# Kernel optimization log

Measured on AMD Instinct MI355X. Metric: run time of the kernel, lower is better.

## Reference

```python
import jax, jax.numpy as jnp
import numpy as np

WS = 7            # window_size
P = WS * WS       # tokens per window
NUM_HEADS = 12
N_SCALES = 3      # n_local_region_scales
LOCAL_HEAD = NUM_HEADS // N_SCALES

# relative position index (Swin-style), precomputed as a constant
_coords = np.stack(np.meshgrid(np.arange(WS), np.arange(WS), indexing='ij'))  # (2,WS,WS)
_cf = _coords.reshape(2, -1)                                                  # (2,P)
_rel = (_cf[:, :, None] - _cf[:, None, :]).transpose(1, 2, 0)                 # (P,P,2)
_rel[:, :, 0] += WS - 1
_rel[:, :, 1] += WS - 1
_rel[:, :, 0] *= 2 * WS - 1
REL_IDX = jnp.asarray(_rel.sum(-1))  # (P,P) int


def window_partition(arr, ws):
    # arr: (B, H, W, C) -> (B * H/ws * W/ws, ws, ws, C)
    B, H, W, C = arr.shape
    a = arr.reshape(B, H // ws, ws, W // ws, ws, C)
    return a.transpose(0, 1, 3, 2, 4, 5).reshape(-1, ws, ws, C)


def setup_inputs() -> dict:
    key = jax.random.key(0)
    ks = jax.random.split(key, 4)
    B, H, W, C = 16, 56, 56, 384
    N = H * W
    return {
        'x': jax.random.normal(ks[0], (B, N, C), dtype=jnp.float32),
        'w_qkv': jax.random.normal(ks[1], (C, 3 * C), dtype=jnp.float32) * 0.02,
        'w_proj': jax.random.normal(ks[2], (C, C), dtype=jnp.float32) * 0.02,
        'b_proj': jnp.zeros((C,), dtype=jnp.float32),
        'rel_bias_table': jax.random.normal(ks[3], ((2 * WS - 1) ** 2, LOCAL_HEAD), dtype=jnp.float32) * 0.02,
        'H': H,
        'W': W,
    }


def reference(x, w_qkv, w_proj, b_proj, rel_bias_table, H, W):
    B, N, C = x.shape
    head_dim = C // NUM_HEADS
    local_C = C // N_SCALES
    scale = head_dim ** -0.5

    # qkv projection (no bias), laid out as (3, B, N, C)
    temp = (x @ w_qkv).reshape(B, N, 3, C).transpose(2, 0, 1, 3)

    # relative position bias: (LOCAL_HEAD, P, P)
    bias = rel_bias_table[REL_IDX.reshape(-1)].reshape(P, P, LOCAL_HEAD).transpose(2, 0, 1)

    outs = []
    for i in range(N_SCALES):
        qkv = temp[:, :, :, i * local_C:(i + 1) * local_C]          # (3,B,N,local_C)
        oh, ow = H // (2 ** i), W // (2 ** i)
        n_region = (oh // WS) * (ow // WS)
        qkv = qkv.reshape(3 * B, N, local_C).transpose(0, 2, 1).reshape(3 * B, local_C, H, W)
        if i > 0:
            k = 2 ** i
            r = qkv.reshape(3 * B, local_C, oh, k, ow, k)
            qkv = r.mean(axis=(3, 5)) + r.max(axis=(3, 5))           # avg_pool + max_pool
        qkv = qkv.transpose(0, 2, 3, 1)                              # (3B, oh, ow, local_C)
        qkv = window_partition(qkv, WS)                              # (3B*n_region, WS, WS, local_C)
        qkv = qkv.reshape(3, B, n_region, WS, WS, LOCAL_HEAD, head_dim).transpose(0, 1, 5, 2, 3, 4, 6)
        # NOTE: the original reshapes (B,LOCAL_HEAD,n_region,WS,WS,hd) -> (-1,LOCAL_HEAD,P,hd),
        # which mixes batch/head/region axes; replicated faithfully (row-major reshape).
        q = qkv[0].reshape(-1, LOCAL_HEAD, P, head_dim)
        kk = qkv[1].reshape(-1, LOCAL_HEAD, P, head_dim)
        v = qkv[2].reshape(-1, LOCAL_HEAD, P, head_dim)
        attn = (q * scale) @ jnp.swapaxes(kk, -2, -1) + bias[None]   # (B*R, LH, P, P)
        attn = jax.nn.softmax(attn, axis=-1)
        y = attn @ v                                                 # (B*R, LH, P, hd)
        # faithful inverse of the mixed reshape + (non-inverse) window merge via plain reshape
        y = y.reshape(B, n_region, LOCAL_HEAD, P, head_dim).transpose(0, 2, 4, 1, 3)
        y = y.reshape(B, local_C, oh, ow)
        if i > 0:
            y = jax.image.resize(y, (B, local_C, H, W), method='bilinear')
        y = y.reshape(B, LOCAL_HEAD, head_dim, H, W).transpose(0, 1, 3, 4, 2)  # (B,LH,H,W,hd)
        outs.append(y)

    fused = jnp.concatenate(outs, axis=1)                            # (B,NUM_HEADS,H,W,hd)
    fused = fused.reshape(B, NUM_HEADS, N, C // NUM_HEADS).transpose(0, 2, 1, 3).reshape(B, N, C)
    return fused @ w_proj + b_proj
```

## Files before the change

kernel.cpp:

```cpp
#include <hip/hip_runtime.h>
#include <hip/hip_bf16.h>

typedef __hip_bfloat16 bf16;
typedef __hip_bfloat162 bf16x2;
typedef __attribute__((ext_vector_type(8))) short short8;
typedef __attribute__((ext_vector_type(4))) float f32x4;

__device__ __forceinline__ void storeOut(float* p, float v) { *p = v; }
__device__ __forceinline__ void storeOut(bf16* p, float v) { *p = __float2bfloat16(v); }

#define GLOAD_LDS16(g, l)                                              \
  __builtin_amdgcn_global_load_lds(                                    \
      (const __attribute__((address_space(1))) void*)(g),              \
      (__attribute__((address_space(3))) void*)(l), 16, 0, 0)

__global__ __launch_bounds__(256) void cvt_f32_bf16_kernel(const float* __restrict__ in,
                                                           bf16* __restrict__ out, int n8)
{
  int i = blockIdx.x * 256 + threadIdx.x;
  if (i >= n8) return;
  const float4* p = (const float4*)in + (size_t)i * 2;
  float4 a = p[0], b = p[1];
  union { short8 v; bf16 h[8]; } u;
  u.h[0] = __float2bfloat16(a.x); u.h[1] = __float2bfloat16(a.y);
  u.h[2] = __float2bfloat16(a.z); u.h[3] = __float2bfloat16(a.w);
  u.h[4] = __float2bfloat16(b.x); u.h[5] = __float2bfloat16(b.y);
  u.h[6] = __float2bfloat16(b.z); u.h[7] = __float2bfloat16(b.w);
  *((short8*)out + i) = u.v;
}

__global__ __launch_bounds__(256) void transpose2_kernel(const float* __restrict__ w_qkv,
                                                         const float* __restrict__ w_proj,
                                                         bf16* __restrict__ wqkvT,
                                                         bf16* __restrict__ wprojT)
{
  int idx = blockIdx.x * 256 + threadIdx.x;
  if (idx < 1152 * 384) {
    int n = idx / 384, k = idx - n * 384;
    wqkvT[idx] = __float2bfloat16(w_qkv[(size_t)k * 1152 + n]);
  } else {
    idx -= 1152 * 384;
    int n = idx / 384, k = idx - n * 384;
    wprojT[idx] = __float2bfloat16(w_proj[(size_t)k * 384 + n]);
  }
}

template<typename TC, bool BIAS>
__global__ __launch_bounds__(256) void gemm_mfma(const bf16* __restrict__ A,
                                                 const bf16* __restrict__ Bt,
                                                 const float* __restrict__ bias,
                                                 TC* __restrict__ C,
                                                 int M, int N, int K, int nbx)
{
  __shared__ __align__(16) bf16 As[2][128 * 64];
  __shared__ __align__(16) bf16 Bs[2][128 * 64];
  const int tid = threadIdx.x;
  const int wave = tid >> 6, lane = tid & 63;
  const int cpx = gridDim.x >> 3;
  const int wg = (blockIdx.x & 7) * cpx + (blockIdx.x >> 3);
  const int by = wg / nbx, bx = wg - by * nbx;
  const int bm = by * 128, bn = bx * 128;
  const int wr = wave >> 1, wc = wave & 1;

  f32x4 acc[4][4] = {};

  const bf16* aP[4];
  const bf16* bP[4];
#pragma unroll
  for (int e = 0; e < 4; ++e) {
    int flat = e * 4096 + tid * 16;
    int r = flat >> 7;
    int q = ((flat >> 4) & 7) ^ (r & 7);
    aP[e] = A + (size_t)(bm + r) * K + q * 8;
    bP[e] = Bt + (size_t)(bn + r) * K + q * 8;
  }

  auto STAGE = [&](int buf, int k0) {
    char* aw = (char*)(&As[buf][0]) + wave * 1024;
    char* bw = (char*)(&Bs[buf][0]) + wave * 1024;
#pragma unroll
    for (int e = 0; e < 4; ++e) {
      GLOAD_LDS16(aP[e] + k0, aw + e * 4096);
      GLOAD_LDS16(bP[e] + k0, bw + e * 4096);
    }
  };

  const int lr = lane & 15, lk = lane >> 4;
  const int rbA = (wr * 64 + lr) * 64;
  const int rbB = (wc * 64 + lr) * 64;
  const int q0 = ((lk    ) ^ (lr & 7)) * 8;
  const int q1 = ((4 + lk) ^ (lr & 7)) * 8;

  const int nt = K >> 6;
  STAGE(0, 0);
  int cur = 0;
  for (int t = 0; t < nt; ++t) {
    __syncthreads();
    if (t + 1 < nt) STAGE(cur ^ 1, (t + 1) << 6);
    const bf16* Ab = &As[cur][0];
    const bf16* Bb = &Bs[cur][0];
    short8 af0[4], af1[4], bf0[4], bf1[4];
#pragma unroll
    for (int i = 0; i < 4; ++i) {
      af0[i] = *(const short8*)(Ab + rbA + i * 1024 + q0);
      af1[i] = *(const short8*)(Ab + rbA + i * 1024 + q1);
    }
#pragma unroll
    for (int j = 0; j < 4; ++j) {
      bf0[j] = *(const short8*)(Bb + rbB + j * 1024 + q0);
      bf1[j] = *(const short8*)(Bb + rbB + j * 1024 + q1);
    }
#pragma unroll
    for (int i = 0; i < 4; ++i)
#pragma unroll
      for (int j = 0; j < 4; ++j) {
        acc[i][j] = __builtin_amdgcn_mfma_f32_16x16x32_bf16(af0[i], bf0[j], acc[i][j], 0, 0, 0);
        acc[i][j] = __builtin_amdgcn_mfma_f32_16x16x32_bf16(af1[i], bf1[j], acc[i][j], 0, 0, 0);
      }
    cur ^= 1;
  }

  const int crow = bm + wr * 64 + lk * 4;
  const int ccol = bn + wc * 64 + lr;
#pragma unroll
  for (int j = 0; j < 4; ++j) {
    int col = ccol + j * 16;
    float bv = BIAS ? bias[col] : 0.f;
#pragma unroll
    for (int i = 0; i < 4; ++i)
#pragma unroll
      for (int t = 0; t < 4; ++t) {
        int row = crow + i * 16 + t;
        storeOut(&C[(size_t)row * N + col], acc[i][j][t] + bv);
      }
  }
}

__global__ __launch_bounds__(128) void pool_both_kernel(const bf16* __restrict__ temp,
                                                        bf16* __restrict__ pool1,
                                                        bf16* __restrict__ pool2)
{
  int blk = blockIdx.x;
  bf16* outp; int oh, k, isc;
  if (blk < 3 * 16 * 28 * 28) { outp = pool1; oh = 28; k = 2; isc = 1; }
  else { blk -= 3 * 16 * 28 * 28; outp = pool2; oh = 14; k = 4; isc = 2; }
  const int ow = oh;
  int c = threadIdx.x;
  int x = blk % ow; int t = blk / ow;
  int y = t % oh;  t /= oh;
  int b = t % 16;  int s = t / 16;
  float sum = 0.f, mx = -3.4e38f;
  float inv = 1.0f / (float)(k * k);
  for (int dy = 0; dy < k; ++dy)
    for (int dx = 0; dx < k; ++dx) {
      int h = y * k + dy, w = x * k + dx;
      float v = __bfloat162float(temp[((size_t)b * 3136 + h * 56 + w) * 1152 + s * 384 + isc * 128 + c]);
      sum += v; mx = fmaxf(mx, v);
    }
  outp[((size_t)(s * 16 + b) * oh * ow + y * ow + x) * 128 + c] = __float2bfloat16(sum * inv + mx);
}

struct AttnP {
  const bf16 *qb, *kb, *vb;
  bf16* out;
  int R, Rw, ow, npos, rstride, out_cstride, out_coffset, blk0;
  long long bstride;
};

__global__ __launch_bounds__(256) void attn_mfma(const float* __restrict__ btable,
                                                 AttnP P0, AttnP P1, AttnP P2)
{
  __shared__ __align__(16) bf16 Kls[4 * 64 * 40];
  __shared__ __align__(16) bf16 Vt[4 * 32 * 64];
  __shared__ __align__(16) bf16 Pls[4 * 64 * 64];
  __shared__ float bias_s[169];

  const AttnP p = (blockIdx.x >= (unsigned)P2.blk0) ? P2
                : (blockIdx.x >= (unsigned)P1.blk0) ? P1 : P0;
  const int blk = blockIdx.x - p.blk0;
  const int b = blk / p.R, r = blk % p.R;
  const int rh = r / p.Rw, rw = r % p.Rw;
  const int tid = threadIdx.x;
  const int h = tid >> 6, lane = tid & 63;
  const int lr = lane & 15, lk = lane >> 4;
  const int hb = r & 3;

  if (tid < 169) bias_s[tid] = btable[tid * 4 + hb];

  const size_t gbase = (size_t)b * p.bstride;

  for (int c = tid; c < 784; c += 256) {
    int hh = c / 196, rem = c - hh * 196;
    int row = rem >> 2, slot = rem & 3;
    int r7 = (row * 9363) >> 16, rm = row - r7 * 7;
    int n = (rh * 7 + r7) * p.ow + rw * 7 + rm;
    short8 v = *(const short8*)(p.kb + gbase + (size_t)n * p.rstride + hh * 32 + slot * 8);
    *(short8*)(Kls + hh * 2560 + row * 40 + slot * 8) = v;
  }
  for (int j = tid; j < 4096; j += 256) {
    int pp = j & 63, dp = (j >> 6) & 15, hh = j >> 10;
    bf16 v0, v1;
    if (pp < 49) {
      int r7 = (pp * 9363) >> 16, rm = pp - r7 * 7;
      int n = (rh * 7 + r7) * p.ow + rw * 7 + rm;
      bf16x2 v2 = *(const bf16x2*)(p.vb + gbase + (size_t)n * p.rstride + hh * 32 + dp * 2);
      v0 = v2.x; v1 = v2.y;
    } else { v0 = __float2bfloat16(0.f); v1 = v0; }
    int d0 = dp * 2, d1 = d0 + 1;
    Vt[hh * 2048 + d0 * 64 + ((pp >> 3) ^ (d0 & 7)) * 8 + (pp & 7)] = v0;
    Vt[hh * 2048 + d1 * 64 + ((pp >> 3) ^ (d1 & 7)) * 8 + (pp & 7)] = v1;
  }

  short8 qa[4];
#pragma unroll
  for (int it = 0; it < 4; ++it) {
    int pq = it * 16 + lr; pq = min(pq, 48);
    int r7 = (pq * 9363) >> 16, rm = pq - r7 * 7;
    int n = (rh * 7 + r7) * p.ow + rw * 7 + rm;
    qa[it] = *(const short8*)(p.qb + gbase + (size_t)n * p.rstride + h * 32 + lk * 8);
  }

  __syncthreads();

  f32x4 s[4][4];
  {
    short8 kf[4];
#pragma unroll
    for (int jt = 0; jt < 4; ++jt)
      kf[jt] = *(const short8*)(Kls + h * 2560 + (jt * 16 + lr) * 40 + lk * 8);
    const f32x4 z = {0.f, 0.f, 0.f, 0.f};
#pragma unroll
    for (int it = 0; it < 4; ++it)
#pragma unroll
      for (int jt = 0; jt < 4; ++jt)
        s[it][jt] = __builtin_amdgcn_mfma_f32_16x16x32_bf16(qa[it], kf[jt], z, 0, 0, 0);
  }

  const float scale = 0.17677669529663687f;
  const bool colpad = (lr != 0);
  int pp7[4], ppm[4];
#pragma unroll
  for (int jt = 0; jt < 4; ++jt) {
    int pp = min(jt * 16 + lr, 48);
    pp7[jt] = (pp * 9363) >> 16; ppm[jt] = pp - pp7[jt] * 7;
  }
  float sm[4][4];
#pragma unroll
  for (int it = 0; it < 4; ++it)
#pragma unroll
    for (int t = 0; t < 4; ++t) {
      int pq = min(it * 16 + lk * 4 + t, 48);
      int q7 = (pq * 9363) >> 16, qm = pq - q7 * 7;
#pragma unroll
      for (int jt = 0; jt < 4; ++jt) {
        float bv = bias_s[(q7 - pp7[jt] + 6) * 13 + (qm - ppm[jt] + 6)];
        float v = fmaf(s[it][jt][t], scale, bv);
        if (jt == 3 && colpad) v = -1e30f;
        s[it][jt][t] = v;
      }
      float m = fmaxf(fmaxf(s[it][0][t], s[it][1][t]), fmaxf(s[it][2][t], s[it][3][t]));
      m = fmaxf(m, __shfl_xor(m, 1));
      m = fmaxf(m, __shfl_xor(m, 2));
      m = fmaxf(m, __shfl_xor(m, 4));
      m = fmaxf(m, __shfl_xor(m, 8));
      float ssum = 0.f;
#pragma unroll
      for (int jt = 0; jt < 4; ++jt) {
        float e = __expf(s[it][jt][t] - m);
        s[it][jt][t] = e; ssum += e;
      }
      ssum += __shfl_xor(ssum, 1);
      ssum += __shfl_xor(ssum, 2);
      ssum += __shfl_xor(ssum, 4);
      ssum += __shfl_xor(ssum, 8);
      sm[it][t] = 1.0f / ssum;
    }

#pragma unroll
  for (int it = 0; it < 4; ++it)
#pragma unroll
    for (int t = 0; t < 4; ++t) {
      int prow = it * 16 + lk * 4 + t;
#pragma unroll
      for (int jt = 0; jt < 4; ++jt) {
        int slot = (jt * 2 + (lr >> 3)) ^ (prow & 7);
        Pls[h * 4096 + prow * 64 + slot * 8 + (lr & 7)] = __float2bfloat16(s[it][jt][t]);
      }
    }
  __syncthreads();

  f32x4 o[4][2] = {};
#pragma unroll
  for (int ks = 0; ks < 2; ++ks) {
    short8 pf[4], vf[2];
#pragma unroll
    for (int it = 0; it < 4; ++it) {
      int prow = it * 16 + lr;
      pf[it] = *(const short8*)(Pls + h * 4096 + prow * 64 + ((ks * 4 + lk) ^ (prow & 7)) * 8);
    }
#pragma unroll
    for (int jd = 0; jd < 2; ++jd) {
      int d = jd * 16 + lr;
      vf[jd] = *(const short8*)(Vt + h * 2048 + d * 64 + ((ks * 4 + lk) ^ (d & 7)) * 8);
    }
#pragma unroll
    for (int it = 0; it < 4; ++it)
#pragma unroll
      for (int jd = 0; jd < 2; ++jd)
        o[it][jd] = __builtin_amdgcn_mfma_f32_16x16x32_bf16(pf[it], vf[jd], o[it][jd], 0, 0, 0);
  }

  const int c0 = (r & 3) * 32;
#pragma unroll
  for (int it = 0; it < 4; ++it)
#pragma unroll
    for (int t = 0; t < 4; ++t) {
      int prow = it * 16 + lk * 4 + t;
      if (prow < 49) {
        int m_out = (h * (p.R >> 2) + (r >> 2)) * 49 + prow;
        bf16* op = p.out + ((size_t)b * p.npos + m_out) * p.out_cstride + p.out_coffset + c0;
#pragma unroll
        for (int jd = 0; jd < 2; ++jd)
          op[jd * 16 + lr] = __float2bfloat16(o[it][jd][t] * sm[it][t]);
      }
    }
}

__device__ __forceinline__ float2 bilerp2(const bf16* __restrict__ base, int dim, int h, int w, int cp)
{
  float r = (float)dim / 56.f;
  float uy = (h + 0.5f) * r - 0.5f;
  float ux = (w + 0.5f) * r - 0.5f;
  float fy0 = floorf(uy), fx0 = floorf(ux);
  int y0 = (int)fy0, x0 = (int)fx0;
  float fy = uy - fy0, fx = ux - fx0;
  int y0c = max(y0, 0), y1c = min(y0 + 1, dim - 1);
  int x0c = max(x0, 0), x1c = min(x0 + 1, dim - 1);
  bf16x2 v00 = *(const bf16x2*)(base + ((size_t)y0c * dim + x0c) * 128 + cp * 2);
  bf16x2 v01 = *(const bf16x2*)(base + ((size_t)y0c * dim + x1c) * 128 + cp * 2);
  bf16x2 v10 = *(const bf16x2*)(base + ((size_t)y1c * dim + x0c) * 128 + cp * 2);
  bf16x2 v11 = *(const bf16x2*)(base + ((size_t)y1c * dim + x1c) * 128 + cp * 2);
  float w00 = (1.f - fy) * (1.f - fx), w01 = (1.f - fy) * fx;
  float w10 = fy * (1.f - fx),        w11 = fy * fx;
  float2 o;
  o.x = w00 * __bfloat162float(v00.x) + w01 * __bfloat162float(v01.x) +
        w10 * __bfloat162float(v10.x) + w11 * __bfloat162float(v11.x);
  o.y = w00 * __bfloat162float(v00.y) + w01 * __bfloat162float(v01.y) +
        w10 * __bfloat162float(v10.y) + w11 * __bfloat162float(v11.y);
  return o;
}

__global__ __launch_bounds__(256) void upsample_both_kernel(const bf16* __restrict__ yb1,
                                                            const bf16* __restrict__ yb2,
                                                            bf16* __restrict__ fused)
{
  int t = blockIdx.x * 256 + threadIdx.x;
  int cp = t & 63;
  int pos = t >> 6;
  int n = pos % 3136, b = pos / 3136;
  int h = n / 56, w = n % 56;
  float2 s1 = bilerp2(yb1 + (size_t)b * 784 * 128, 28, h, w, cp);
  float2 s2 = bilerp2(yb2 + (size_t)b * 196 * 128, 14, h, w, cp);
  bf16* op = fused + (size_t)pos * 384;
  bf16x2 o1; o1.x = __float2bfloat16(s1.x); o1.y = __float2bfloat16(s1.y);
  bf16x2 o2; o2.x = __float2bfloat16(s2.x); o2.y = __float2bfloat16(s2.y);
  *(bf16x2*)(op + 128 + cp * 2) = o1;
  *(bf16x2*)(op + 256 + cp * 2) = o2;
}

extern "C" void kernel_launch(void* const* d_in, const int* in_sizes, int n_in,
                              void* d_out, int out_size, void* d_ws, size_t ws_size,
                              hipStream_t stream)
{
  const float* x      = (const float*)d_in[0];
  const float* w_qkv  = (const float*)d_in[1];
  const float* w_proj = (const float*)d_in[2];
  const float* b_proj = (const float*)d_in[3];
  const float* btable = (const float*)d_in[4];

  bf16* temp  = (bf16*)d_ws;
  bf16* pool1 = temp  + (size_t)50176 * 1152;
  bf16* pool2 = pool1 + (size_t)3 * 16 * 784 * 128;
  bf16* fused = pool2 + (size_t)3 * 16 * 196 * 128;
  bf16* ybuf1 = fused + (size_t)50176 * 384;
  bf16* ybuf2 = ybuf1 + (size_t)16 * 784 * 128;
  bf16* wqkvT = ybuf2 + (size_t)16 * 196 * 128;
  bf16* wprojT= wqkvT + (size_t)1152 * 384;
  bf16* xb    = fused;

  cvt_f32_bf16_kernel<<<(50176 * 384 / 8 + 255) / 256, 256, 0, stream>>>(x, xb, 50176 * 384 / 8);
  transpose2_kernel<<<(1152 * 384 + 384 * 384) / 256, 256, 0, stream>>>(w_qkv, w_proj, wqkvT, wprojT);

  gemm_mfma<bf16, false><<<3528, 256, 0, stream>>>(
      xb, wqkvT, nullptr, temp, 50176, 1152, 384, 9);

  pool_both_kernel<<<3 * 16 * 28 * 28 + 3 * 16 * 14 * 14, 128, 0, stream>>>(temp, pool1, pool2);

  AttnP P0{temp, temp + 384, temp + 768, fused,
           64, 8, 56, 3136, 1152, 384, 0, 0, (long long)3136 * 1152};
  AttnP P1{pool1, pool1 + (size_t)16 * 784 * 128, pool1 + (size_t)2 * 16 * 784 * 128, ybuf1,
           16, 4, 28, 784, 128, 128, 0, 1024, (long long)784 * 128};
  AttnP P2{pool2, pool2 + (size_t)16 * 196 * 128, pool2 + (size_t)2 * 16 * 196 * 128, ybuf2,
           4, 2, 14, 196, 128, 128, 0, 1280, (long long)196 * 128};
  attn_mfma<<<1344, 256, 0, stream>>>(btable, P0, P1, P2);

  upsample_both_kernel<<<16 * 3136 * 64 / 256, 256, 0, stream>>>(ybuf1, ybuf2, fused);

  gemm_mfma<float, true><<<1176, 256, 0, stream>>>(
      fused, wprojT, b_proj, (float*)d_out, 50176, 384, 384, 3);
}
```

Measured before the change: 210.2 us.

## Merge prep kernels, single-buffer GEMM LDS, alias attention P with K, add setprio

Merges the x conversion and weight transpose into one prep launch. Drops double buffering in the MFMA GEMM so LDS use halves, aiming for higher occupancy at the cost of an extra barrier and less load/compute overlap. The attention kernel reuses the K tile buffer for the probability matrix to cut LDS footprint, and raises wave priority around the MFMA sections.

```diff
diff --git a/kernel.cpp b/kernel.cpp
--- a/kernel.cpp
+++ b/kernel.cpp
@@ -14,34 +14,34 @@
       (const __attribute__((address_space(1))) void*)(g),              \
       (__attribute__((address_space(3))) void*)(l), 16, 0, 0)
 
-__global__ __launch_bounds__(256) void cvt_f32_bf16_kernel(const float* __restrict__ in,
-                                                           bf16* __restrict__ out, int n8)
-{
-  int i = blockIdx.x * 256 + threadIdx.x;
-  if (i >= n8) return;
-  const float4* p = (const float4*)in + (size_t)i * 2;
-  float4 a = p[0], b = p[1];
-  union { short8 v; bf16 h[8]; } u;
-  u.h[0] = __float2bfloat16(a.x); u.h[1] = __float2bfloat16(a.y);
-  u.h[2] = __float2bfloat16(a.z); u.h[3] = __float2bfloat16(a.w);
-  u.h[4] = __float2bfloat16(b.x); u.h[5] = __float2bfloat16(b.y);
-  u.h[6] = __float2bfloat16(b.z); u.h[7] = __float2bfloat16(b.w);
-  *((short8*)out + i) = u.v;
-}
-
-__global__ __launch_bounds__(256) void transpose2_kernel(const float* __restrict__ w_qkv,
-                                                         const float* __restrict__ w_proj,
-                                                         bf16* __restrict__ wqkvT,
-                                                         bf16* __restrict__ wprojT)
-{
-  int idx = blockIdx.x * 256 + threadIdx.x;
-  if (idx < 1152 * 384) {
-    int n = idx / 384, k = idx - n * 384;
-    wqkvT[idx] = __float2bfloat16(w_qkv[(size_t)k * 1152 + n]);
+__global__ __launch_bounds__(256) void prep_kernel(const float* __restrict__ x,
+                                                   const float* __restrict__ w_qkv,
+                                                   const float* __restrict__ w_proj,
+                                                   bf16* __restrict__ xb,
+                                                   bf16* __restrict__ wqkvT,
+                                                   bf16* __restrict__ wprojT)
+{
+  int bid = blockIdx.x;
+  if (bid < 9408) {
+    int i = bid * 256 + threadIdx.x;
+    const float4* p = (const float4*)x + (size_t)i * 2;
+    float4 a = p[0], b = p[1];
+    union { short8 v; bf16 h[8]; } u;
+    u.h[0] = __float2bfloat16(a.x); u.h[1] = __float2bfloat16(a.y);
+    u.h[2] = __float2bfloat16(a.z); u.h[3] = __float2bfloat16(a.w);
+    u.h[4] = __float2bfloat16(b.x); u.h[5] = __float2bfloat16(b.y);
+    u.h[6] = __float2bfloat16(b.z); u.h[7] = __float2bfloat16(b.w);
+    *((short8*)xb + i) = u.v;
   } else {
-    idx -= 1152 * 384;
-    int n = idx / 384, k = idx - n * 384;
-    wprojT[idx] = __float2bfloat16(w_proj[(size_t)k * 384 + n]);
+    int idx = (bid - 9408) * 256 + threadIdx.x;
+    if (idx < 1152 * 384) {
+      int n = idx / 384, k = idx - n * 384;
+      wqkvT[idx] = __float2bfloat16(w_qkv[(size_t)k * 1152 + n]);
+    } else {
+      idx -= 1152 * 384;
+      int n = idx / 384, k = idx - n * 384;
+      wprojT[idx] = __float2bfloat16(w_proj[(size_t)k * 384 + n]);
+    }
   }
 }
 
@@ -52,8 +52,8 @@
                                                  TC* __restrict__ C,
                                                  int M, int N, int K, int nbx)
 {
-  __shared__ __align__(16) bf16 As[2][128 * 64];
-  __shared__ __align__(16) bf16 Bs[2][128 * 64];
+  __shared__ __align__(16) bf16 As[128 * 64];
+  __shared__ __align__(16) bf16 Bs[128 * 64];
   const int tid = threadIdx.x;
   const int wave = tid >> 6, lane = tid & 63;
   const int cpx = gridDim.x >> 3;
@@ -74,16 +74,8 @@
     aP[e] = A + (size_t)(bm + r) * K + q * 8;
     bP[e] = Bt + (size_t)(bn + r) * K + q * 8;
   }
-
-  auto STAGE = [&](int buf, int k0) {
-    char* aw = (char*)(&As[buf][0]) + wave * 1024;
-    char* bw = (char*)(&Bs[buf][0]) + wave * 1024;
-#pragma unroll
-    for (int e = 0; e < 4; ++e) {
-      GLOAD_LDS16(aP[e] + k0, aw + e * 4096);
-      GLOAD_LDS16(bP[e] + k0, bw + e * 4096);
-    }
-  };
+  char* AsW = (char*)As + wave * 1024;
+  char* BsW = (char*)Bs + wave * 1024;
 
   const int lr = lane & 15, lk = lane >> 4;
   const int rbA = (wr * 64 + lr) * 64;
@@ -91,24 +83,22 @@
   const int q0 = ((lk    ) ^ (lr & 7)) * 8;
   const int q1 = ((4 + lk) ^ (lr & 7)) * 8;
 
-  const int nt = K >> 6;
-  STAGE(0, 0);
-  int cur = 0;
-  for (int t = 0; t < nt; ++t) {
+  for (int k0 = 0; k0 < K; k0 += 64) {
+#pragma unroll
+    for (int e = 0; e < 4; ++e) GLOAD_LDS16(aP[e] + k0, AsW + e * 4096);
+#pragma unroll
+    for (int e = 0; e < 4; ++e) GLOAD_LDS16(bP[e] + k0, BsW + e * 4096);
     __syncthreads();
-    if (t + 1 < nt) STAGE(cur ^ 1, (t + 1) << 6);
-    const bf16* Ab = &As[cur][0];
-    const bf16* Bb = &Bs[cur][0];
     short8 af0[4], af1[4], bf0[4], bf1[4];
 #pragma unroll
     for (int i = 0; i < 4; ++i) {
-      af0[i] = *(const short8*)(Ab + rbA + i * 1024 + q0);
-      af1[i] = *(const short8*)(Ab + rbA + i * 1024 + q1);
+      af0[i] = *(const short8*)(As + rbA + i * 1024 + q0);
+      af1[i] = *(const short8*)(As + rbA + i * 1024 + q1);
     }
 #pragma unroll
     for (int j = 0; j < 4; ++j) {
-      bf0[j] = *(const short8*)(Bb + rbB + j * 1024 + q0);
-      bf1[j] = *(const short8*)(Bb + rbB + j * 1024 + q1);
+      bf0[j] = *(const short8*)(Bs + rbB + j * 1024 + q0);
+      bf1[j] = *(const short8*)(Bs + rbB + j * 1024 + q1);
     }
 #pragma unroll
     for (int i = 0; i < 4; ++i)
@@ -117,7 +107,7 @@
         acc[i][j] = __builtin_amdgcn_mfma_f32_16x16x32_bf16(af0[i], bf0[j], acc[i][j], 0, 0, 0);
         acc[i][j] = __builtin_amdgcn_mfma_f32_16x16x32_bf16(af1[i], bf1[j], acc[i][j], 0, 0, 0);
       }
-    cur ^= 1;
+    __syncthreads();
   }
 
   const int crow = bm + wr * 64 + lk * 4;
@@ -170,9 +160,8 @@
 __global__ __launch_bounds__(256) void attn_mfma(const float* __restrict__ btable,
                                                  AttnP P0, AttnP P1, AttnP P2)
 {
-  __shared__ __align__(16) bf16 Kls[4 * 64 * 40];
-  __shared__ __align__(16) bf16 Vt[4 * 32 * 64];
-  __shared__ __align__(16) bf16 Pls[4 * 64 * 64];
+  __shared__ __align__(16) bf16 KP[4 * 4096];
+  __shared__ __align__(16) bf16 Vt[4 * 2048];
   __shared__ float bias_s[169];
 
   const AttnP p = (blockIdx.x >= (unsigned)P2.blk0) ? P2
@@ -195,7 +184,7 @@
     int r7 = (row * 9363) >> 16, rm = row - r7 * 7;
     int n = (rh * 7 + r7) * p.ow + rw * 7 + rm;
     short8 v = *(const short8*)(p.kb + gbase + (size_t)n * p.rstride + hh * 32 + slot * 8);
-    *(short8*)(Kls + hh * 2560 + row * 40 + slot * 8) = v;
+    *(short8*)(KP + hh * 4096 + row * 40 + slot * 8) = v;
   }
   for (int j = tid; j < 4096; j += 256) {
     int pp = j & 63, dp = (j >> 6) & 15, hh = j >> 10;
@@ -227,13 +216,15 @@
     short8 kf[4];
 #pragma unroll
     for (int jt = 0; jt < 4; ++jt)
-      kf[jt] = *(const short8*)(Kls + h * 2560 + (jt * 16 + lr) * 40 + lk * 8);
+      kf[jt] = *(const short8*)(KP + h * 4096 + (jt * 16 + lr) * 40 + lk * 8);
     const f32x4 z = {0.f, 0.f, 0.f, 0.f};
+    __builtin_amdgcn_s_setprio(1);
 #pragma unroll
     for (int it = 0; it < 4; ++it)
 #pragma unroll
       for (int jt = 0; jt < 4; ++jt)
         s[it][jt] = __builtin_amdgcn_mfma_f32_16x16x32_bf16(qa[it], kf[jt], z, 0, 0, 0);
+    __builtin_amdgcn_s_setprio(0);
   }
 
   const float scale = 0.17677669529663687f;
@@ -284,7 +275,7 @@
 #pragma unroll
       for (int jt = 0; jt < 4; ++jt) {
         int slot = (jt * 2 + (lr >> 3)) ^ (prow & 7);
-        Pls[h * 4096 + prow * 64 + slot * 8 + (lr & 7)] = __float2bfloat16(s[it][jt][t]);
+        KP[h * 4096 + prow * 64 + slot * 8 + (lr & 7)] = __float2bfloat16(s[it][jt][t]);
       }
     }
   __syncthreads();
@@ -296,18 +287,20 @@
 #pragma unroll
     for (int it = 0; it < 4; ++it) {
       int prow = it * 16 + lr;
-      pf[it] = *(const short8*)(Pls + h * 4096 + prow * 64 + ((ks * 4 + lk) ^ (prow & 7)) * 8);
+      pf[it] = *(const short8*)(KP + h * 4096 + prow * 64 + ((ks * 4 + lk) ^ (prow & 7)) * 8);
     }
 #pragma unroll
     for (int jd = 0; jd < 2; ++jd) {
       int d = jd * 16 + lr;
       vf[jd] = *(const short8*)(Vt + h * 2048 + d * 64 + ((ks * 4 + lk) ^ (d & 7)) * 8);
     }
+    __builtin_amdgcn_s_setprio(1);
 #pragma unroll
     for (int it = 0; it < 4; ++it)
 #pragma unroll
       for (int jd = 0; jd < 2; ++jd)
         o[it][jd] = __builtin_amdgcn_mfma_f32_16x16x32_bf16(pf[it], vf[jd], o[it][jd], 0, 0, 0);
+    __builtin_amdgcn_s_setprio(0);
   }
 
   const int c0 = (r & 3) * 32;
@@ -388,8 +381,7 @@
   bf16* wprojT= wqkvT + (size_t)1152 * 384;
   bf16* xb    = fused;
 
-  cvt_f32_bf16_kernel<<<(50176 * 384 / 8 + 255) / 256, 256, 0, stream>>>(x, xb, 50176 * 384 / 8);
-  transpose2_kernel<<<(1152 * 384 + 384 * 384) / 256, 256, 0, stream>>>(w_qkv, w_proj, wqkvT, wprojT);
+  prep_kernel<<<9408 + 2304, 256, 0, stream>>>(x, w_qkv, w_proj, xb, wqkvT, wprojT);
 
   gemm_mfma<bf16, false><<<3528, 256, 0, stream>>>(
       xb, wqkvT, nullptr, temp, 50176, 1152, 384, 9);
```

Result: no change. 206.7 us (-1.7%).
